# Optimization experiments

Measured on AMD Instinct MI355X. Metric: run time of the kernel, lower is better.

## Reference

```python
import jax, jax.numpy as jnp
import numpy as np

B, NH, S, H = 4, 8, 1024, 128
I = 512
E = 8
K = 2
EPS = 1e-5


def setup_inputs() -> dict:
    key = jax.random.key(0)
    ks = jax.random.split(key, 11)
    sH = 1.0 / np.sqrt(H)
    sI = 1.0 / np.sqrt(I)
    return {
        "x": jax.random.normal(ks[0], (B, NH, S, H), dtype=jnp.float32),
        "gate_w": jax.random.uniform(ks[1], (E, H), jnp.float32, -sH, sH),
        "gate_b": jax.random.uniform(ks[2], (E,), jnp.float32, -sH, sH),
        "ln1_g": jnp.ones((E, H), jnp.float32),
        "ln1_b": jnp.zeros((E, H), jnp.float32),
        "w1": jax.random.uniform(ks[3], (E, I, H), jnp.float32, -sH, sH),
        "ln2_g": jnp.ones((E, I), jnp.float32),
        "ln2_b": jnp.zeros((E, I), jnp.float32),
        "w2": jax.random.uniform(ks[4], (E, H, I), jnp.float32, -sI, sI),
        "b2": jax.random.uniform(ks[5], (E, H), jnp.float32, -sI, sI),
    }


def _ln_normalize(x):
    mu = jnp.mean(x, axis=-1, keepdims=True)
    var = jnp.mean(jnp.square(x - mu), axis=-1, keepdims=True)
    return (x - mu) * jax.lax.rsqrt(var + EPS)


def reference(x, gate_w, gate_b, ln1_g, ln1_b, w1, ln2_g, ln2_b, w2, b2):
    orig_shape = x.shape
    x_flat = x.reshape(-1, H)  # [N, H]

    # gate: softmax over experts, then top-k
    logits = x_flat @ gate_w.T + gate_b  # [N, E]
    probs = jax.nn.softmax(logits, axis=-1)
    topk_scores, topk_idx = jax.lax.top_k(probs, K)  # [N, K]

    # per-expert MLP (dropout is identity in eval). Normalization of x is
    # expert-independent; affine params differ per expert.
    xn = _ln_normalize(x_flat)  # [N, H]
    h1 = xn[None, :, :] * ln1_g[:, None, :] + ln1_b[:, None, :]  # [E, N, H]
    a1 = jax.nn.gelu(h1, approximate=False)
    t = jnp.einsum("enh,eih->eni", a1, w1)  # [E, N, I]
    h2 = _ln_normalize(t) * ln2_g[:, None, :] + ln2_b[:, None, :]
    a2 = jax.nn.gelu(h2, approximate=False)
    expert_out = jnp.einsum("eni,ehi->enh", a2, w2) + b2[:, None, :]  # [E, N, H]

    # combine weights: sum top-k scores into dense [N, E]
    combine = jnp.sum(jax.nn.one_hot(topk_idx, E, dtype=x.dtype) * topk_scores[..., None], axis=1)
    out = jnp.einsum("ne,enh->nh", combine, expert_out)
    return out.reshape(orig_shape)
```

## Files before the change

kernel.cpp:

```cpp
#include <hip/hip_runtime.h>

#define N_TOK 32768
#define H 128
#define I_DIM 512
#define E 8
#define EPS 1e-5f
#define GATE_TPB 128
#define NSLOT_MAX (N_TOK * 2 + E * 32)

typedef __attribute__((ext_vector_type(8))) short short8;
typedef __attribute__((ext_vector_type(4))) float f32x4;
typedef __attribute__((ext_vector_type(2))) unsigned int u32x2;
typedef __attribute__((ext_vector_type(8))) __bf16 bf16x8;

__device__ inline unsigned short f2bf(float f){
  unsigned int u = __builtin_bit_cast(unsigned int, f);
  u += 0x7fffu + ((u >> 16) & 1u);
  return (unsigned short)(u >> 16);
}
__device__ inline float bf2f(unsigned short s){
  unsigned int u = ((unsigned int)s) << 16;
  return __builtin_bit_cast(float, u);
}
__device__ inline unsigned int pack2(float a, float b){
  return (unsigned int)f2bf(a) | ((unsigned int)f2bf(b) << 16);
}
__device__ inline float gelu_fast(float x){
  const float A = 0.10294517f;
  const float B = 2.30214175f;
  float x2 = x * x;
  float v  = __builtin_fmaf(x2, A, B);
  float z  = __builtin_amdgcn_exp2f(v * x);
  float r  = __builtin_amdgcn_rcpf(z + 1.f);
  return __builtin_fmaf(-x, r, x);
}
__device__ inline f32x4 mfma16(short8 a, short8 b, f32x4 c){
  return __builtin_amdgcn_mfma_f32_16x16x32_bf16(
      __builtin_bit_cast(bf16x8, a), __builtin_bit_cast(bf16x8, b), c, 0, 0, 0);
}

__device__ inline int slot_to_expert(const int* __restrict__ cnt, int slot0,
                                     int& base, int& ne){
  int e = -1, p = 0;
  #pragma unroll
  for (int q = 0; q < E; ++q){
    int c = cnt[q];
    int pc = (c + 31) & ~31;
    if (slot0 >= p && slot0 < p + pc){ e = q; base = slot0 - p; ne = c; }
    p += pc;
  }
  return e;
}

__global__ __launch_bounds__(256) void k_front(
    const float* __restrict__ w1, const float* __restrict__ w2,
    unsigned short* __restrict__ w1p, unsigned short* __restrict__ w2p,
    const float* __restrict__ x, const float* __restrict__ gw,
    const float* __restrict__ gb, unsigned short* __restrict__ xn,
    int* __restrict__ cnt, int* __restrict__ list, float* __restrict__ score,
    float* __restrict__ out){
  __shared__ __align__(16) float gws[E * H];
  __shared__ float gbs[E];
  __shared__ int   lcnt[E];
  __shared__ int   gbase[E];
  __shared__ int   te[2][GATE_TPB];
  __shared__ float tsc[2][GATE_TPB];
  __shared__ int   tlp[2][GATE_TPB];

  int tid = threadIdx.x;
  int blk = blockIdx.x;

  if (blk >= 512){
    float4 z = {0.f, 0.f, 0.f, 0.f};
    float4* o4 = (float4*)out;
    int base4 = (blk - 512) * 2048 + tid;
    #pragma unroll
    for (int q = 0; q < 8; ++q) o4[base4 + q * 256] = z;
    return;
  }

  if (blk < 256){
    int q = blk * 256 + tid;
    int e = q >> 13, rem = q & 8191;
    {
      int it = rem >> 8, kt = (rem >> 6) & 3, l = rem & 63;
      int row = it * 16 + (l & 15), h0 = kt * 32 + (l >> 4) * 8;
      const float* src = w1 + ((size_t)(e * 512 + row) * 128 + h0);
      float4 v0 = *(const float4*)src, v1 = *(const float4*)(src + 4);
      short8 o;
      #pragma unroll
      for (int j = 0; j < 4; ++j){ o[j] = (short)f2bf(v0[j]); o[j+4] = (short)f2bf(v1[j]); }
      *(short8*)(w1p + (size_t)q * 8) = o;
    }
    {
      int ht = rem >> 10, kt = (rem >> 6) & 15, l = rem & 63;
      int row = ht * 16 + (l & 15), i0 = kt * 32 + (l >> 4) * 8;
      const float* src = w2 + ((size_t)(e * 128 + row) * 512 + i0);
      float4 v0 = *(const float4*)src, v1 = *(const float4*)(src + 4);
      short8 o;
      #pragma unroll
      for (int j = 0; j < 4; ++j){ o[j] = (short)f2bf(v0[j]); o[j+4] = (short)f2bf(v1[j]); }
      *(short8*)(w2p + (size_t)q * 8) = o;
    }
    return;
  }

  for (int i = tid; i < E * H; i += 256) gws[i] = gw[i];
  if (tid < E){ gbs[tid] = gb[tid]; lcnt[tid] = 0; }
  __syncthreads();

  int wave = tid >> 6, lane = tid & 63;
  int g = lane >> 3, c8 = lane & 7;
  int tok0 = (blk - 256) * GATE_TPB;
  const float4* gws4 = (const float4*)gws;

  for (int t = 0; t < 4; ++t){
    int lt = t * 32 + wave * 8 + g;
    int tok = tok0 + lt;
    const float4* xr = (const float4*)(x + (size_t)tok * H) + c8 * 4;
    float4 v[4];
    #pragma unroll
    for (int q = 0; q < 4; ++q) v[q] = xr[q];

    float S = 0.f, Q = 0.f;
    float lg[E];
    #pragma unroll
    for (int e = 0; e < E; e++) lg[e] = 0.f;
    #pragma unroll
    for (int q = 0; q < 4; ++q){
      #pragma unroll
      for (int r = 0; r < 4; ++r){
        float f = v[q][r];
        S += f; Q = __builtin_fmaf(f, f, Q);
      }
      #pragma unroll
      for (int e = 0; e < E; e++){
        float4 wv = gws4[e * 32 + c8 * 4 + q];
        #pragma unroll
        for (int r = 0; r < 4; ++r) lg[e] = __builtin_fmaf(v[q][r], wv[r], lg[e]);
      }
    }
    #pragma unroll
    for (int m = 1; m < 8; m <<= 1){
      S += __shfl_xor(S, m);
      Q += __shfl_xor(Q, m);
      #pragma unroll
      for (int e = 0; e < E; e++) lg[e] += __shfl_xor(lg[e], m);
    }

    float mu = S * (1.f / H);
    float var = Q * (1.f / H) - mu * mu;
    float rsig = rsqrtf(fmaxf(var, 0.f) + EPS);

    short8 s0, s1;
    #pragma unroll
    for (int r = 0; r < 4; ++r){
      s0[r]     = (short)f2bf((v[0][r] - mu) * rsig);
      s0[r + 4] = (short)f2bf((v[1][r] - mu) * rsig);
      s1[r]     = (short)f2bf((v[2][r] - mu) * rsig);
      s1[r + 4] = (short)f2bf((v[3][r] - mu) * rsig);
    }
    unsigned short* xo = xn + (size_t)tok * H + c8 * 16;
    *(short8*)xo = s0;
    *(short8*)(xo + 8) = s1;

    if (c8 == 0){
      float mx = -1e30f;
      #pragma unroll
      for (int e = 0; e < E; e++){ lg[e] += gbs[e]; mx = fmaxf(mx, lg[e]); }
      float p[E], sum = 0.f;
      #pragma unroll
      for (int e = 0; e < E; e++){ p[e] = __expf(lg[e] - mx); sum += p[e]; }
      float inv = 1.f / sum;
      int e0 = 0; float p0 = p[0];
      #pragma unroll
      for (int e = 1; e < E; e++) if (p[e] > p0){ e0 = e; p0 = p[e]; }
      int e1 = -1; float p1 = -1.f;
      #pragma unroll
      for (int e = 0; e < E; e++) if (e != e0 && p[e] > p1){ e1 = e; p1 = p[e]; }
      te[0][lt] = e0; tsc[0][lt] = p0 * inv; tlp[0][lt] = atomicAdd(&lcnt[e0], 1);
      te[1][lt] = e1; tsc[1][lt] = p1 * inv; tlp[1][lt] = atomicAdd(&lcnt[e1], 1);
    }
  }
  __syncthreads();
  if (tid < E) gbase[tid] = atomicAdd(&cnt[tid], lcnt[tid]);
  __syncthreads();
  if (tid < GATE_TPB){
    int tok = tok0 + tid;
    #pragma unroll
    for (int k2 = 0; k2 < 2; k2++){
      int ee = te[k2][tid];
      int pos = gbase[ee] + tlp[k2][tid];
      list[ee * N_TOK + pos] = tok;
      score[ee * N_TOK + pos] = tsc[k2][tid];
    }
  }
}

__global__ __launch_bounds__(256, 2) void k_mlp(
    const unsigned short* __restrict__ xn,
    const float* __restrict__ ln1g, const float* __restrict__ ln1b,
    const unsigned short* __restrict__ w1p,
    const float* __restrict__ ln2g, const float* __restrict__ ln2b,
    const unsigned short* __restrict__ w2p, const float* __restrict__ b2,
    const int* __restrict__ cnt, const int* __restrict__ list,
    const float* __restrict__ score, float* __restrict__ out){
  __shared__ __align__(16) unsigned short tls[2][16 * I_DIM];
  __shared__ float2 psum[4][2][16];
  __shared__ __align__(16) float pg2[I_DIM], pb2[I_DIM];
  __shared__ float pbb[H];

  int tid = threadIdx.x, wv = tid >> 6, lane = tid & 63;
  int slot0 = blockIdx.x * 32;
  int base, ne;
  int e = slot_to_expert(cnt, slot0, base, ne);
  if (e < 0 || base >= ne) return;
  const int l15 = lane & 15, l4 = lane >> 4;

  pg2[tid]       = ln2g[e * I_DIM + tid];
  pg2[tid + 256] = ln2g[e * I_DIM + tid + 256];
  pb2[tid]       = ln2b[e * I_DIM + tid];
  pb2[tid + 256] = ln2b[e * I_DIM + tid + 256];
  if (tid < H) pbb[tid] = b2[e * H + tid];

  {
    const float* g1e = ln1g + e * H;
    const float* b1e = ln1b + e * H;
    #pragma unroll
    for (int c2 = 0; c2 < 2; ++c2){
      int combo = wv * 2 + c2;
      int kt = combo >> 1, tl = combo & 1;
      int h0 = kt * 32 + l4 * 8;
      int s = base + tl * 16 + l15;
      int tok = s < ne ? list[e * N_TOK + s] : 0;
      short8 xv = *(const short8*)(xn + (size_t)tok * H + h0);
      float4 ga = *(const float4*)(g1e + h0), gbv = *(const float4*)(g1e + h0 + 4);
      float4 ba = *(const float4*)(b1e + h0), bbv = *(const float4*)(b1e + h0 + 4);
      short8 o;
      #pragma unroll
      for (int j = 0; j < 8; ++j){
        float f = bf2f((unsigned short)xv[j]);
        float gg = j < 4 ? ga[j] : gbv[j - 4];
        float bb_ = j < 4 ? ba[j] : bbv[j - 4];
        o[j] = (short)f2bf(gelu_fast(__builtin_fmaf(f, gg, bb_)));
      }
      *(short8*)((char*)&tls[0][0] + (size_t)((combo * 64 + lane) << 4)) = o;
    }
  }
  __syncthreads();
  short8 b1f[4][2];
  #pragma unroll
  for (int kt = 0; kt < 4; ++kt)
    #pragma unroll
    for (int tl = 0; tl < 2; ++tl)
      b1f[kt][tl] = *(const short8*)((const char*)&tls[0][0] +
                                     (size_t)(((kt * 2 + tl) * 64 + lane) << 4));
  __syncthreads();

  const unsigned short* w1e = w1p + ((size_t)e << 16);
  float Sx[2] = {0.f, 0.f}, Qx[2] = {0.f, 0.f};

  #pragma unroll
  for (int ii = 0; ii < 8; ++ii){
    int it = wv * 8 + ii;
    short8 af[4];
    #pragma unroll
    for (int kt = 0; kt < 4; ++kt)
      af[kt] = *(const short8*)(w1e + (size_t)(((it << 2) | kt) << 9) + lane * 8);
    f32x4 acc[2];
    #pragma unroll
    for (int tl = 0; tl < 2; ++tl){ f32x4 z = {0.f,0.f,0.f,0.f}; acc[tl] = z; }
    #pragma unroll
    for (int kt = 0; kt < 4; ++kt)
      #pragma unroll
      for (int tl = 0; tl < 2; ++tl)
        acc[tl] = mfma16(af[kt], b1f[kt][tl], acc[tl]);

    int kt2 = it >> 1;
    int lh = (it * 2 + (l4 >> 1)) & 3;
    int off = ((kt2 * 4 + lh) * 16 + l15) * 8 + (l4 & 1) * 4;
    #pragma unroll
    for (int tl = 0; tl < 2; ++tl){
      #pragma unroll
      for (int r = 0; r < 4; ++r){
        float v = acc[tl][r];
        Sx[tl] += v; Qx[tl] = __builtin_fmaf(v, v, Qx[tl]);
      }
      u32x2 w0;
      w0[0] = pack2(acc[tl][0], acc[tl][1]);
      w0[1] = pack2(acc[tl][2], acc[tl][3]);
      *(u32x2*)((char*)&tls[tl][0] + (size_t)off * 2) = w0;
    }
  }

  #pragma unroll
  for (int tl = 0; tl < 2; ++tl){
    Sx[tl] += __shfl_xor(Sx[tl], 16);  Qx[tl] += __shfl_xor(Qx[tl], 16);
    Sx[tl] += __shfl_xor(Sx[tl], 32);  Qx[tl] += __shfl_xor(Qx[tl], 32);
  }
  if (l4 == 0){
    #pragma unroll
    for (int tl = 0; tl < 2; ++tl)
      psum[wv][tl][l15] = make_float2(Sx[tl], Qx[tl]);
  }
  __syncthreads();

  {
    int tl3 = wv & 1, ktb = (wv >> 1) * 8;
    float S = 0.f, Q = 0.f;
    #pragma unroll
    for (int w4 = 0; w4 < 4; ++w4){
      float2 p = psum[w4][tl3][l15];
      S += p.x; Q += p.y;
    }
    float mu = S * (1.f / I_DIM);
    float var = __builtin_fmaf(Q, 1.f / I_DIM, -mu * mu);
    float rsig = rsqrtf(fmaxf(var, 0.f) + EPS);
    float mrs = mu * rsig;

    unsigned short* ta = &tls[tl3][0];
    #pragma unroll
    for (int k2 = 0; k2 < 8; ++k2){
      int kt = ktb + k2;
      int i0 = kt * 32 + l4 * 8;
      float4 g2a = *(const float4*)(pg2 + i0), g2b = *(const float4*)(pg2 + i0 + 4);
      float4 b2a = *(const float4*)(pb2 + i0), b2b = *(const float4*)(pb2 + i0 + 4);
      short8 tv = *(const short8*)((const char*)ta + (size_t)(kt * 64 + lane) * 16);
      short8 f0;
      #pragma unroll
      for (int j = 0; j < 8; ++j){
        float gg = j < 4 ? g2a[j] : g2b[j - 4];
        float bb_ = j < 4 ? b2a[j] : b2b[j - 4];
        float v0 = __builtin_fmaf(bf2f((unsigned short)tv[j]), rsig, -mrs);
        f0[j] = (short)f2bf(gelu_fast(__builtin_fmaf(v0, gg, bb_)));
      }
      *(short8*)((char*)ta + (size_t)(kt * 64 + lane) * 16) = f0;
    }
  }
  __syncthreads();

  const unsigned short* w2e = w2p + ((size_t)e << 16);
  f32x4 c[2][2];
  #pragma unroll
  for (int hh = 0; hh < 2; ++hh)
    #pragma unroll
    for (int tl = 0; tl < 2; ++tl){ f32x4 z = {0.f,0.f,0.f,0.f}; c[hh][tl] = z; }

  #pragma unroll
  for (int kt = 0; kt < 16; ++kt){
    short8 aw[2];
    #pragma unroll
    for (int hh = 0; hh < 2; ++hh){
      int h = wv * 2 + hh;
      aw[hh] = *(const short8*)(w2e + (size_t)(((h << 4) | kt) << 9) + lane * 8);
    }
    #pragma unroll
    for (int tl = 0; tl < 2; ++tl){
      short8 f0 = *(const short8*)((const char*)&tls[tl][0] +
                                   (size_t)(kt * 64 + lane) * 16);
      c[0][tl] = mfma16(f0, aw[0], c[0][tl]);
      c[1][tl] = mfma16(f0, aw[1], c[1][tl]);
    }
  }

  float bb[2];
  #pragma unroll
  for (int hh = 0; hh < 2; ++hh) bb[hh] = pbb[(wv * 2 + hh) * 16 + l15];

  #pragma unroll
  for (int tl = 0; tl < 2; ++tl){
    #pragma unroll
    for (int r = 0; r < 4; ++r){
      int s = base + tl * 16 + l4 * 4 + r;
      if (s < ne){
        int tok = list[e * N_TOK + s];
        float sc = score[e * N_TOK + s];
        float* orow = out + (size_t)tok * H + l15;
        #pragma unroll
        for (int hh = 0; hh < 2; ++hh)
          atomicAdd(orow + (wv * 2 + hh) * 16, (c[hh][tl][r] + bb[hh]) * sc);
      }
    }
  }
}

extern "C" void kernel_launch(void* const* d_in, const int* in_sizes, int n_in,
                              void* d_out, int out_size, void* d_ws, size_t ws_size,
                              hipStream_t stream){
  const float* x     = (const float*)d_in[0];
  const float* gw    = (const float*)d_in[1];
  const float* gb    = (const float*)d_in[2];
  const float* ln1g  = (const float*)d_in[3];
  const float* ln1b  = (const float*)d_in[4];
  const float* w1    = (const float*)d_in[5];
  const float* ln2g  = (const float*)d_in[6];
  const float* ln2b  = (const float*)d_in[7];
  const float* w2    = (const float*)d_in[8];
  const float* b2    = (const float*)d_in[9];
  float* out = (float*)d_out;

  char* w = (char*)d_ws;
  unsigned short* xn  = (unsigned short*)w;  w += (size_t)N_TOK * H * 2;
  unsigned short* w1p = (unsigned short*)w;  w += (size_t)E * I_DIM * H * 2;
  unsigned short* w2p = (unsigned short*)w;  w += (size_t)E * H * I_DIM * 2;
  int*    list  = (int*)w;                   w += (size_t)E * N_TOK * 4;
  float*  score = (float*)w;                 w += (size_t)E * N_TOK * 4;
  int*    cnt   = (int*)w;                   w += 256;

  hipMemsetAsync(cnt, 0, 256, stream);

  k_front<<<dim3(1024), dim3(256), 0, stream>>>(
      w1, w2, w1p, w2p, x, gw, gb, xn, cnt, list, score, out);
  k_mlp<<<dim3(NSLOT_MAX / 32), dim3(256), 0, stream>>>(
      xn, ln1g, ln1b, w1p, ln2g, ln2b, w2p, b2, cnt, list, score, out);
}
```

Baseline: 75.60 us.

## Double-buffer weight fragment loads and use packed bf16 conversion in MLP kernel

Both GEMM loops in the expert MLP kernel now prefetch the next iteration's weight (and LDS activation) fragments into a second register buffer while the current MFMAs run. The MFMA blocks are wrapped in s_setprio to raise wave priority. The manual round-to-nearest bf16 packing is replaced by the HIP float2-to-bfloat162 conversion, which can lower to a packed convert instruction. The extra buffers raise register pressure and may reduce occupancy, and the compiler may already have been scheduling these loads early.

```diff
diff --git a/kernel.cpp b/kernel.cpp
--- a/kernel.cpp
+++ b/kernel.cpp
@@ -1,4 +1,5 @@
 #include <hip/hip_runtime.h>
+#include <hip/hip_bf16.h>
 
 #define N_TOK 32768
 #define H 128
@@ -11,6 +12,7 @@
 typedef __attribute__((ext_vector_type(8))) short short8;
 typedef __attribute__((ext_vector_type(4))) float f32x4;
 typedef __attribute__((ext_vector_type(2))) unsigned int u32x2;
+typedef __attribute__((ext_vector_type(4))) unsigned int u32x4;
 typedef __attribute__((ext_vector_type(8))) __bf16 bf16x8;
 
 __device__ inline unsigned short f2bf(float f){
@@ -22,8 +24,11 @@
   unsigned int u = ((unsigned int)s) << 16;
   return __builtin_bit_cast(float, u);
 }
-__device__ inline unsigned int pack2(float a, float b){
-  return (unsigned int)f2bf(a) | ((unsigned int)f2bf(b) << 16);
+__device__ inline unsigned int cvtpk(float lo, float hi){
+  __hip_bfloat162 h = __float22bfloat162_rn(make_float2(lo, hi));
+  unsigned int r;
+  __builtin_memcpy(&r, &h, 4);
+  return r;
 }
 __device__ inline float gelu_fast(float x){
   const float A = 0.10294517f;
@@ -236,15 +241,18 @@
       short8 xv = *(const short8*)(xn + (size_t)tok * H + h0);
       float4 ga = *(const float4*)(g1e + h0), gbv = *(const float4*)(g1e + h0 + 4);
       float4 ba = *(const float4*)(b1e + h0), bbv = *(const float4*)(b1e + h0 + 4);
-      short8 o;
+      float q[8];
       #pragma unroll
       for (int j = 0; j < 8; ++j){
         float f = bf2f((unsigned short)xv[j]);
         float gg = j < 4 ? ga[j] : gbv[j - 4];
         float bb_ = j < 4 ? ba[j] : bbv[j - 4];
-        o[j] = (short)f2bf(gelu_fast(__builtin_fmaf(f, gg, bb_)));
-      }
-      *(short8*)((char*)&tls[0][0] + (size_t)((combo * 64 + lane) << 4)) = o;
+        q[j] = gelu_fast(__builtin_fmaf(f, gg, bb_));
+      }
+      u32x4 vw;
+      vw[0] = cvtpk(q[0], q[1]); vw[1] = cvtpk(q[2], q[3]);
+      vw[2] = cvtpk(q[4], q[5]); vw[3] = cvtpk(q[6], q[7]);
+      *(u32x4*)((char*)&tls[0][0] + (size_t)((combo * 64 + lane) << 4)) = vw;
     }
   }
   __syncthreads();
@@ -260,21 +268,32 @@
   const unsigned short* w1e = w1p + ((size_t)e << 16);
   float Sx[2] = {0.f, 0.f}, Qx[2] = {0.f, 0.f};
 
+  short8 afA[4], afB[4];
+  {
+    int it = wv * 8;
+    #pragma unroll
+    for (int kt = 0; kt < 4; ++kt)
+      afA[kt] = *(const short8*)(w1e + (size_t)(((it << 2) | kt) << 9) + lane * 8);
+  }
   #pragma unroll
   for (int ii = 0; ii < 8; ++ii){
     int it = wv * 8 + ii;
-    short8 af[4];
+    if (ii < 7){
+      int itn = it + 1;
+      #pragma unroll
+      for (int kt = 0; kt < 4; ++kt)
+        afB[kt] = *(const short8*)(w1e + (size_t)(((itn << 2) | kt) << 9) + lane * 8);
+    }
+    f32x4 acc[2];
+    #pragma unroll
+    for (int tl = 0; tl < 2; ++tl){ f32x4 z = {0.f,0.f,0.f,0.f}; acc[tl] = z; }
+    __builtin_amdgcn_s_setprio(1);
     #pragma unroll
     for (int kt = 0; kt < 4; ++kt)
-      af[kt] = *(const short8*)(w1e + (size_t)(((it << 2) | kt) << 9) + lane * 8);
-    f32x4 acc[2];
-    #pragma unroll
-    for (int tl = 0; tl < 2; ++tl){ f32x4 z = {0.f,0.f,0.f,0.f}; acc[tl] = z; }
-    #pragma unroll
-    for (int kt = 0; kt < 4; ++kt)
       #pragma unroll
       for (int tl = 0; tl < 2; ++tl)
-        acc[tl] = mfma16(af[kt], b1f[kt][tl], acc[tl]);
+        acc[tl] = mfma16(afA[kt], b1f[kt][tl], acc[tl]);
+    __builtin_amdgcn_s_setprio(0);
 
     int kt2 = it >> 1;
     int lh = (it * 2 + (l4 >> 1)) & 3;
@@ -287,10 +306,12 @@
         Sx[tl] += v; Qx[tl] = __builtin_fmaf(v, v, Qx[tl]);
       }
       u32x2 w0;
-      w0[0] = pack2(acc[tl][0], acc[tl][1]);
-      w0[1] = pack2(acc[tl][2], acc[tl][3]);
+      w0[0] = cvtpk(acc[tl][0], acc[tl][1]);
+      w0[1] = cvtpk(acc[tl][2], acc[tl][3]);
       *(u32x2*)((char*)&tls[tl][0] + (size_t)off * 2) = w0;
     }
+    #pragma unroll
+    for (int kt = 0; kt < 4; ++kt) afA[kt] = afB[kt];
   }
 
   #pragma unroll
@@ -326,15 +347,18 @@
       float4 g2a = *(const float4*)(pg2 + i0), g2b = *(const float4*)(pg2 + i0 + 4);
       float4 b2a = *(const float4*)(pb2 + i0), b2b = *(const float4*)(pb2 + i0 + 4);
       short8 tv = *(const short8*)((const char*)ta + (size_t)(kt * 64 + lane) * 16);
-      short8 f0;
+      float q[8];
       #pragma unroll
       for (int j = 0; j < 8; ++j){
         float gg = j < 4 ? g2a[j] : g2b[j - 4];
         float bb_ = j < 4 ? b2a[j] : b2b[j - 4];
         float v0 = __builtin_fmaf(bf2f((unsigned short)tv[j]), rsig, -mrs);
-        f0[j] = (short)f2bf(gelu_fast(__builtin_fmaf(v0, gg, bb_)));
-      }
-      *(short8*)((char*)ta + (size_t)(kt * 64 + lane) * 16) = f0;
+        q[j] = gelu_fast(__builtin_fmaf(v0, gg, bb_));
+      }
+      u32x4 vw;
+      vw[0] = cvtpk(q[0], q[1]); vw[1] = cvtpk(q[2], q[3]);
+      vw[2] = cvtpk(q[4], q[5]); vw[3] = cvtpk(q[6], q[7]);
+      *(u32x4*)((char*)ta + (size_t)(kt * 64 + lane) * 16) = vw;
     }
   }
   __syncthreads();
@@ -346,21 +370,41 @@
     #pragma unroll
     for (int tl = 0; tl < 2; ++tl){ f32x4 z = {0.f,0.f,0.f,0.f}; c[hh][tl] = z; }
 
-  #pragma unroll
-  for (int kt = 0; kt < 16; ++kt){
-    short8 aw[2];
+  short8 awA[2], awB[2], fA[2], fB[2];
+  {
     #pragma unroll
     for (int hh = 0; hh < 2; ++hh){
       int h = wv * 2 + hh;
-      aw[hh] = *(const short8*)(w2e + (size_t)(((h << 4) | kt) << 9) + lane * 8);
-    }
+      awA[hh] = *(const short8*)(w2e + (size_t)(((h << 4) | 0) << 9) + lane * 8);
+    }
+    #pragma unroll
+    for (int tl = 0; tl < 2; ++tl)
+      fA[tl] = *(const short8*)((const char*)&tls[tl][0] + (size_t)(0 * 64 + lane) * 16);
+  }
+  #pragma unroll
+  for (int kt = 0; kt < 16; ++kt){
+    if (kt < 15){
+      int ktn = kt + 1;
+      #pragma unroll
+      for (int hh = 0; hh < 2; ++hh){
+        int h = wv * 2 + hh;
+        awB[hh] = *(const short8*)(w2e + (size_t)(((h << 4) | ktn) << 9) + lane * 8);
+      }
+      #pragma unroll
+      for (int tl = 0; tl < 2; ++tl)
+        fB[tl] = *(const short8*)((const char*)&tls[tl][0] + (size_t)(ktn * 64 + lane) * 16);
+    }
+    __builtin_amdgcn_s_setprio(1);
     #pragma unroll
     for (int tl = 0; tl < 2; ++tl){
-      short8 f0 = *(const short8*)((const char*)&tls[tl][0] +
-                                   (size_t)(kt * 64 + lane) * 16);
-      c[0][tl] = mfma16(f0, aw[0], c[0][tl]);
-      c[1][tl] = mfma16(f0, aw[1], c[1][tl]);
-    }
+      c[0][tl] = mfma16(fA[tl], awA[0], c[0][tl]);
+      c[1][tl] = mfma16(fA[tl], awA[1], c[1][tl]);
+    }
+    __builtin_amdgcn_s_setprio(0);
+    #pragma unroll
+    for (int hh = 0; hh < 2; ++hh) awA[hh] = awB[hh];
+    #pragma unroll
+    for (int tl = 0; tl < 2; ++tl) fA[tl] = fB[tl];
   }
 
   float bb[2];
@@ -407,7 +451,7 @@
   float*  score = (float*)w;                 w += (size_t)E * N_TOK * 4;
   int*    cnt   = (int*)w;                   w += 256;
 
-  hipMemsetAsync(cnt, 0, 256, stream);
+  (void)hipMemsetAsync(cnt, 0, 256, stream);
 
   k_front<<<dim3(1024), dim3(256), 0, stream>>>(
       w1, w2, w1p, w2p, x, gw, gb, xn, cnt, list, score, out);
```

Result: faster. 73.90 us (-2.3%).
